# Kernel tuning notes

Hardware: AMD Instinct MI355X
Metric: run time of the kernel (lower is better)

The kernel has to match this reference:

```python
import jax, jax.numpy as jnp
import numpy as np

B, H, W = 4, 64, 64
DIM, NH, HD = 768, 12, 64
MLP_DIM = 3072
WS = 14
EPS = 1e-6
SCALE = HD ** -0.5
QMIN, QMAX = -128.0, 127.0  # 8-bit signed fake-quant range


def fake_quant(x, s):
    # uniform quant-dequant with straight-through estimator
    q = jnp.clip(jnp.round(x / s), QMIN, QMAX) * s
    return x + jax.lax.stop_gradient(q - x)


def layer_norm(x, w, b):
    mu = jnp.mean(x, axis=-1, keepdims=True)
    var = jnp.var(x, axis=-1, keepdims=True)
    return (x - mu) * jax.lax.rsqrt(var + EPS) * w + b


def qlinear(x, w, b, a_s, w_s):
    # PreQuantizedLayer: fake-quant input activation and weight, then linear
    return fake_quant(x, a_s) @ fake_quant(w, w_s).T + b


def _attention(xw, qkv_w, qkv_b, proj_w, proj_b, rel_pos_h, rel_pos_w, a_s, w_s):
    Bw = xw.shape[0]
    N = WS * WS
    qkv = qlinear(xw.reshape(Bw, N, DIM), qkv_w, qkv_b, a_s[4], w_s[0])
    qkv = qkv.reshape(Bw, N, 3, NH, HD).transpose(2, 0, 3, 1, 4).reshape(3, Bw * NH, N, HD)
    q = fake_quant(qkv[0], a_s[0])
    k = fake_quant(qkv[1], a_s[1])
    v = fake_quant(qkv[2], a_s[2])
    attn = jnp.einsum('bqc,bkc->bqk', q * SCALE, k)  # (Bw*NH, N, N)
    # decomposed relative position bias (q_size == k_size == WS)
    idx = jnp.arange(WS)[:, None] - jnp.arange(WS)[None, :] + (WS - 1)
    Rh = rel_pos_h[idx]  # (WS, WS, HD)
    Rw = rel_pos_w[idx]
    r_q = q.reshape(Bw * NH, WS, WS, HD)
    rel_h = jnp.einsum('bhwc,hkc->bhwk', r_q, Rh)
    rel_w = jnp.einsum('bhwc,wkc->bhwk', r_q, Rw)
    attn = (attn.reshape(-1, WS, WS, WS, WS) + rel_h[..., :, None] + rel_w[..., None, :]).reshape(-1, N, N)
    attn = fake_quant(jax.nn.softmax(attn, axis=-1), a_s[3])
    out = jnp.einsum('bqk,bkc->bqc', attn, v)
    out = out.reshape(Bw, NH, WS, WS, HD).transpose(0, 2, 3, 1, 4).reshape(Bw, WS, WS, DIM)
    return qlinear(out, proj_w, proj_b, a_s[5], w_s[1])


def _forward(x, ln1_w, ln1_b, ln2_w, ln2_b, qkv_w, qkv_b, proj_w, proj_b,
             lin1_w, lin1_b, lin2_w, lin2_b, rel_pos_h, rel_pos_w, act_scales, w_scales):
    shortcut = x
    h = layer_norm(x, ln1_w, ln1_b)
    pad_h = (WS - H % WS) % WS
    pad_w = (WS - W % WS) % WS
    Hp, Wp = H + pad_h, W + pad_w
    hp = jnp.pad(h, ((0, 0), (0, pad_h), (0, pad_w), (0, 0)))
    win = hp.reshape(B, Hp // WS, WS, Wp // WS, WS, DIM).transpose(0, 1, 3, 2, 4, 5).reshape(-1, WS, WS, DIM)
    win = _attention(win, qkv_w, qkv_b, proj_w, proj_b, rel_pos_h, rel_pos_w, act_scales, w_scales)
    hp = win.reshape(B, Hp // WS, Wp // WS, WS, WS, DIM).transpose(0, 1, 3, 2, 4, 5).reshape(B, Hp, Wp, DIM)
    x = shortcut + hp[:, :H, :W, :]
    y = layer_norm(x, ln2_w, ln2_b)
    y = qlinear(y, lin1_w, lin1_b, act_scales[6], w_scales[2])
    y = jax.nn.gelu(y, approximate=False)
    y = qlinear(y, lin2_w, lin2_b, act_scales[7], w_scales[3])
    return x + y


def setup_inputs() -> dict:
    key = jax.random.key(0)
    ks = jax.random.split(key, 12)
    def w(k, shape, std=0.02):
        return jax.random.normal(k, shape, dtype=jnp.float32) * std
    return {
        'x': jax.random.normal(ks[0], (B, H, W, DIM), dtype=jnp.float32),
        'ln1_w': jnp.ones((DIM,), jnp.float32), 'ln1_b': jnp.zeros((DIM,), jnp.float32),
        'ln2_w': jnp.ones((DIM,), jnp.float32), 'ln2_b': jnp.zeros((DIM,), jnp.float32),
        'qkv_w': w(ks[1], (3 * DIM, DIM)), 'qkv_b': jnp.zeros((3 * DIM,), jnp.float32),
        'proj_w': w(ks[2], (DIM, DIM)), 'proj_b': jnp.zeros((DIM,), jnp.float32),
        'lin1_w': w(ks[3], (MLP_DIM, DIM)), 'lin1_b': jnp.zeros((MLP_DIM,), jnp.float32),
        'lin2_w': w(ks[4], (DIM, MLP_DIM)), 'lin2_b': jnp.zeros((DIM,), jnp.float32),
        'rel_pos_h': w(ks[5], (2 * WS - 1, HD)), 'rel_pos_w': w(ks[6], (2 * WS - 1, HD)),
        'act_scales': jax.random.uniform(ks[7], (8,), jnp.float32, 0.01, 0.06),
        'w_scales': jax.random.uniform(ks[8], (4,), jnp.float32, 0.0005, 0.003),
    }


def reference(x, ln1_w, ln1_b, ln2_w, ln2_b, qkv_w, qkv_b, proj_w, proj_b,
              lin1_w, lin1_b, lin2_w, lin2_b, rel_pos_h, rel_pos_w, act_scales, w_scales):
    return _forward(x, ln1_w, ln1_b, ln2_w, ln2_b, qkv_w, qkv_b, proj_w, proj_b,
                    lin1_w, lin1_b, lin2_w, lin2_b, rel_pos_h, rel_pos_w, act_scales, w_scales)
```

## Files before the change

kernel.cpp:

```cpp
#include <hip/hip_runtime.h>
#include <cstdint>


typedef int   v4i __attribute__((ext_vector_type(4)));
typedef float v4f __attribute__((ext_vector_type(4)));
typedef short v8s __attribute__((ext_vector_type(8)));
typedef int8_t i8;

__device__ __forceinline__ i8 satq(float x) {
  float q = rintf(x);
  q = fminf(127.f, fmaxf(-128.f, q));
  return (i8)(int)q;
}

__device__ __forceinline__ void gload16(const i8* g, i8* l) {
  __builtin_amdgcn_global_load_lds((const __attribute__((address_space(1))) void*)g,
                                   (__attribute__((address_space(3))) void*)l, 16, 0, 0);
}

__device__ __forceinline__ int pack4(const i8* q) {
  return ((int)(unsigned char)q[0]) | ((int)(unsigned char)q[1] << 8) |
         ((int)(unsigned char)q[2] << 16) | ((int)(unsigned char)q[3] << 24);
}

__device__ __forceinline__ float fast_gelu(float v) {
  float x = fabsf(v) * 0.70710678118654752f;
  float t = __builtin_amdgcn_rcpf(fmaf(0.3275911f, x, 1.0f));
  float s = fmaf(1.061405429f, t, -1.453152027f);
  s = fmaf(s, t, 1.421413741f);
  s = fmaf(s, t, -0.284496736f);
  s = fmaf(s, t, 0.254829592f);
  s = s * t;
  float e = __expf(-x * x);
  float erfa = fmaf(-s, e, 1.0f);
  float erfs = copysignf(erfa, v);
  float hv = 0.5f * v;
  return fmaf(hv, erfs, hv);
}

__global__ __launch_bounds__(256) void k_prep(const float* __restrict__ qkvw,
    const float* __restrict__ projw, const float* __restrict__ lin1w,
    const float* __restrict__ lin2w, i8* __restrict__ wqb,
    const float* __restrict__ rph, const float* __restrict__ rpw,
    short* __restrict__ TB, const float* __restrict__ wsc) {
  int b = blockIdx.x;
  if (b < 1728) {
    int i = b * 256 + threadIdx.x;
    const float* w; int base, sidx;
    if (i < 110592)      { w = qkvw;  base = 0;      sidx = 0; }
    else if (i < 147456) { w = projw; base = 110592; sidx = 1; }
    else if (i < 294912) { w = lin1w; base = 147456; sidx = 2; }
    else                 { w = lin2w; base = 294912; sidx = 3; }
    float inv = 1.0f / wsc[sidx];
    const float4* src = (const float4*)w + (size_t)(i - base) * 4;
    i8 buf[16];
#pragma unroll
    for (int t = 0; t < 4; t++) {
      float4 f = src[t];
      buf[t*4+0] = satq(f.x * inv); buf[t*4+1] = satq(f.y * inv);
      buf[t*4+2] = satq(f.z * inv); buf[t*4+3] = satq(f.w * inv);
    }
    *(v4i*)(wqb + (size_t)i * 16) = *(v4i*)buf;
  } else {
    int g = (b - 1728) * 256 + threadIdx.x;
    int lane = g & 63, c = g >> 6;
    int p = c & 1, ks = (c >> 1) & 1, nt = (c >> 2) & 1, tb = c >> 3;
    const float* src = tb ? rpw : rph;
    int n = nt * 16 + (lane & 15);
    int k0 = ks * 32 + (lane >> 4) * 8;
    short outv[8];
#pragma unroll
    for (int j = 0; j < 8; j++) {
      float v = (n < 27) ? src[n * 64 + k0 + j] : 0.f;
      unsigned u = __float_as_uint(v);
      unsigned hi = (u + 0x7fffu + ((u >> 16) & 1u)) >> 16;
      if (p == 0) outv[j] = (short)hi;
      else {
        float lof = v - __uint_as_float(hi << 16);
        unsigned ul = __float_as_uint(lof);
        outv[j] = (short)((ul + 0x7fffu + ((ul >> 16) & 1u)) >> 16);
      }
    }
    *(v8s*)(TB + (size_t)c * 512 + lane * 8) = *(v8s*)outv;
  }
}

__global__ __launch_bounds__(256) void k_ln1(const float* __restrict__ x,
    const float* __restrict__ w, const float* __restrict__ b,
    const float* __restrict__ as, i8* __restrict__ outq) {
  int wt = blockIdx.x * 4 + (threadIdx.x >> 6);
  int lane = threadIdx.x & 63;
  int win = wt / 196, tok = wt - win * 196;
  int bb = win / 25, wrem = win - bb * 25, wh = wrem / 5, ww = wrem - wh * 5;
  int r = tok / 14, c = tok - r * 14;
  int y = wh * 14 + r, xx = ww * 14 + c;
  i8* dst = outq + (size_t)wt * 768 + lane * 12;
  if (y >= 64 || xx >= 64) {
    ((int*)dst)[0] = 0; ((int*)dst)[1] = 0; ((int*)dst)[2] = 0;
    return;
  }
  const float* row = x + (((size_t)bb * 64 + y) * 64 + xx) * 768 + lane * 12;
  float v[12];
  *(float4*)(v)     = *(const float4*)(row);
  *(float4*)(v + 4) = *(const float4*)(row + 4);
  *(float4*)(v + 8) = *(const float4*)(row + 8);
  float s = 0.f, ss = 0.f;
#pragma unroll
  for (int j = 0; j < 12; j++) { s += v[j]; ss += v[j] * v[j]; }
#pragma unroll
  for (int off = 1; off < 64; off <<= 1) { s += __shfl_xor(s, off); ss += __shfl_xor(ss, off); }
  float mu = s * (1.0f / 768.0f);
  float var = ss * (1.0f / 768.0f) - mu * mu;
  float rstd = 1.0f / sqrtf(var + 1e-6f);
  float inv = 1.0f / as[4];
  float wv[12], bv[12];
  *(float4*)(wv)     = *(const float4*)(w + lane * 12);
  *(float4*)(wv + 4) = *(const float4*)(w + lane * 12 + 4);
  *(float4*)(wv + 8) = *(const float4*)(w + lane * 12 + 8);
  *(float4*)(bv)     = *(const float4*)(b + lane * 12);
  *(float4*)(bv + 4) = *(const float4*)(b + lane * 12 + 4);
  *(float4*)(bv + 8) = *(const float4*)(b + lane * 12 + 8);
  i8 q[12];
#pragma unroll
  for (int j = 0; j < 12; j++) q[j] = satq(((v[j] - mu) * rstd * wv[j] + bv[j]) * inv);
  ((int*)dst)[0] = pack4(q); ((int*)dst)[1] = pack4(q + 4); ((int*)dst)[2] = pack4(q + 8);
}

__global__ __launch_bounds__(256) void k_ln2(const float* __restrict__ x2,
    const float* __restrict__ w, const float* __restrict__ b,
    const float* __restrict__ as, i8* __restrict__ outq) {
  int tokg = blockIdx.x * 4 + (threadIdx.x >> 6);
  int lane = threadIdx.x & 63;
  const float* row = x2 + (size_t)tokg * 768 + lane * 12;
  float v[12];
  *(float4*)(v)     = *(const float4*)(row);
  *(float4*)(v + 4) = *(const float4*)(row + 4);
  *(float4*)(v + 8) = *(const float4*)(row + 8);
  float s = 0.f, ss = 0.f;
#pragma unroll
  for (int j = 0; j < 12; j++) { s += v[j]; ss += v[j] * v[j]; }
#pragma unroll
  for (int off = 1; off < 64; off <<= 1) { s += __shfl_xor(s, off); ss += __shfl_xor(ss, off); }
  float mu = s * (1.0f / 768.0f);
  float var = ss * (1.0f / 768.0f) - mu * mu;
  float rstd = 1.0f / sqrtf(var + 1e-6f);
  float inv = 1.0f / as[6];
  float wv[12], bv[12];
  *(float4*)(wv)     = *(const float4*)(w + lane * 12);
  *(float4*)(wv + 4) = *(const float4*)(w + lane * 12 + 4);
  *(float4*)(wv + 8) = *(const float4*)(w + lane * 12 + 8);
  *(float4*)(bv)     = *(const float4*)(b + lane * 12);
  *(float4*)(bv + 4) = *(const float4*)(b + lane * 12 + 4);
  *(float4*)(bv + 8) = *(const float4*)(b + lane * 12 + 8);
  i8* dst = outq + (size_t)tokg * 768 + lane * 12;
  i8 q[12];
#pragma unroll
  for (int j = 0; j < 12; j++) q[j] = satq(((v[j] - mu) * rstd * wv[j] + bv[j]) * inv);
  ((int*)dst)[0] = pack4(q); ((int*)dst)[1] = pack4(q + 4); ((int*)dst)[2] = pack4(q + 8);
}

template <class Epi>
__global__ __launch_bounds__(256) void k_gemm(const i8* __restrict__ A, const i8* __restrict__ B,
                                              int M, int N, int K, Epi epi) {
  __shared__ __align__(16) i8 As[3][8192];
  __shared__ __align__(16) i8 Bs[3][8192];
  const int tid = threadIdx.x;
  const int lane = tid & 63, wave = tid >> 6;
  const int quad = lane >> 4, lc = lane & 15;
  const int wr = wave >> 1, wc = wave & 1;
  const long bm = (long)blockIdx.y * 128, bn = (long)blockIdx.x * 128;
  const v4i vz = {0, 0, 0, 0};
  v4i acc[4][4];
#pragma unroll
  for (int i = 0; i < 4; i++)
#pragma unroll
    for (int j = 0; j < 4; j++) acc[i][j] = vz;

  const int r0 = tid >> 2, c0 = tid & 3;
  const int cs = c0 ^ ((r0 >> 1) & 3);
  long rA0 = bm + r0;      if (rA0 >= M) rA0 = 0;
  long rA1 = bm + r0 + 64; if (rA1 >= M) rA1 = 0;
  const i8* pA0 = A + rA0 * (size_t)K + cs * 16;
  const i8* pA1 = A + rA1 * (size_t)K + cs * 16;
  const i8* pB0 = B + (bn + r0)      * (size_t)K + cs * 16;
  const i8* pB1 = B + (bn + r0 + 64) * (size_t)K + cs * 16;

  auto stage = [&](int buf) {
    gload16(pA0, As[buf] + tid * 16); gload16(pA1, As[buf] + 4096 + tid * 16);
    gload16(pB0, Bs[buf] + tid * 16); gload16(pB1, Bs[buf] + 4096 + tid * 16);
    pA0 += 64; pA1 += 64; pB0 += 64; pB1 += 64;
  };

  const int xq16 = (quad ^ ((lc >> 1) & 3)) * 16;

  auto compute = [&](int buf) {
    v4i af[4], bf[4];
#pragma unroll
    for (int i = 0; i < 4; i++) af[i] = *(const v4i*)(As[buf] + (wr * 64 + i * 16 + lc) * 64 + xq16);
#pragma unroll
    for (int j = 0; j < 4; j++) bf[j] = *(const v4i*)(Bs[buf] + (wc * 64 + j * 16 + lc) * 64 + xq16);
#pragma unroll
    for (int i = 0; i < 4; i++)
#pragma unroll
      for (int j = 0; j < 4; j++)
        acc[i][j] = __builtin_amdgcn_mfma_i32_16x16x64_i8(bf[j], af[i], acc[i][j], 0, 0, 0);
  };

  const int nt = K >> 6;
  stage(0); stage(1);
  int cb = 0, sb = 2;
  for (int t = 0; t < nt - 1; ++t) {
    asm volatile("s_waitcnt vmcnt(4)" ::: "memory");
    __builtin_amdgcn_s_barrier();
    asm volatile("" ::: "memory");
    if (t + 2 < nt) { stage(sb); if (++sb == 3) sb = 0; }
    compute(cb); if (++cb == 3) cb = 0;
  }
  asm volatile("s_waitcnt vmcnt(0)" ::: "memory");
  __builtin_amdgcn_s_barrier();
  asm volatile("" ::: "memory");
  compute(cb);

  Epi e = epi;
  e.init();
#pragma unroll
  for (int i = 0; i < 4; i++) {
    int gm = (int)bm + wr * 64 + i * 16 + lc;
#pragma unroll
    for (int j = 0; j < 4; j++) {
      int gn0 = (int)bn + wc * 64 + j * 16 + quad * 4;
      if (gm < M) e.store4(acc[i][j], gm, gn0);
    }
  }
}

struct EpiQKV {
  const float* as; const float* wsc; const float* bias;
  i8 *qq, *kq, *vt;
  float sab, invq, invk, invv;
  __device__ void init() {
    sab = as[4] * wsc[0]; invq = 1.f / as[0]; invk = 1.f / as[1]; invv = 1.f / as[2];
  }
  __device__ void store4(const v4i a, int m, int n0) {
    int t = n0 / 768, rem = n0 - t * 768;
    int head = rem >> 6, ch0 = rem & 63;
    int win = m / 196, tok = m - win * 196;
    size_t bh = (size_t)win * 12 + head;
    float4 bv = *(const float4*)(bias + n0);
    const float* bp = (const float*)&bv;
    if (t == 2) {
#pragma unroll
      for (int r = 0; r < 4; r++)
        vt[(bh * 64 + ch0 + r) * 256 + tok] = satq(((float)a[r] * sab + bp[r]) * invv);
    } else {
      float inv = (t == 0) ? invq : invk;
      i8 q[4];
#pragma unroll
      for (int r = 0; r < 4; r++) q[r] = satq(((float)a[r] * sab + bp[r]) * inv);
      *(int*)((t == 0 ? qq : kq) + (bh * 196 + tok) * 64 + ch0) = pack4(q);
    }
  }
};

struct EpiProj {
  const float* as; const float* wsc; const float* bias; const float* x0; float* out;
  float sab;
  __device__ void init() { sab = as[5] * wsc[1]; }
  __device__ void store4(const v4i a, int m, int n0) {
    int win = m / 196, tok = m - win * 196;
    int bb = win / 25, wrem = win - bb * 25, wh = wrem / 5, ww = wrem - wh * 5;
    int rr = tok / 14, cc = tok - rr * 14;
    int y = wh * 14 + rr, xx = ww * 14 + cc;
    if (y >= 64 || xx >= 64) return;
    size_t o = (((size_t)bb * 64 + y) * 64 + xx) * 768 + n0;
    float4 bv = *(const float4*)(bias + n0);
    float4 xv = *(const float4*)(x0 + o);
    float4 ov;
    ov.x = (float)a[0] * sab + bv.x + xv.x;
    ov.y = (float)a[1] * sab + bv.y + xv.y;
    ov.z = (float)a[2] * sab + bv.z + xv.z;
    ov.w = (float)a[3] * sab + bv.w + xv.w;
    *(float4*)(out + o) = ov;
  }
};

struct EpiLin1 {
  const float* as; const float* wsc; const float* bias; i8* outq;
  float sab, invg;
  __device__ void init() { sab = as[6] * wsc[2]; invg = 1.f / as[7]; }
  __device__ void store4(const v4i a, int m, int n0) {
    float4 bv = *(const float4*)(bias + n0);
    const float* bp = (const float*)&bv;
    i8 q[4];
#pragma unroll
    for (int r = 0; r < 4; r++) {
      float v = fmaf((float)a[r], sab, bp[r]);
      q[r] = satq(fast_gelu(v) * invg);
    }
    *(int*)(outq + (size_t)m * 3072 + n0) = pack4(q);
  }
};

struct EpiLin2 {
  const float* as; const float* wsc; const float* bias; float* out;
  float sab;
  __device__ void init() { sab = as[7] * wsc[3]; }
  __device__ void store4(const v4i a, int m, int n0) {
    size_t o = (size_t)m * 768 + n0;
    float4 bv = *(const float4*)(bias + n0);
    float4 ov = *(const float4*)(out + o);
    ov.x += (float)a[0] * sab + bv.x;
    ov.y += (float)a[1] * sab + bv.y;
    ov.z += (float)a[2] * sab + bv.z;
    ov.w += (float)a[3] * sab + bv.w;
    *(float4*)(out + o) = ov;
  }
};

__global__ __launch_bounds__(64, 4) void k_attn(const i8* __restrict__ qq, const i8* __restrict__ kq,
    const i8* __restrict__ vt, const short* __restrict__ TB,
    const float* __restrict__ as, i8* __restrict__ outq) {
  __shared__ float relS[16][66];
  const int g = blockIdx.x;
  const int work = (g & 7) * 1950 + (g >> 3);
  const int bh = work / 13;
  const int t = work - bh * 13;
  const int win = bh / 12, head = bh - win * 12;
  const int lane = threadIdx.x;
  const int quad = lane >> 4, lc = lane & 15;
  const float s0 = as[0];
  const float ssc = s0 * as[1] * 0.125f;
  const float invs3 = 1.0f / as[3];
  const float oscale = as[2] * as[3] / as[5];

  const v8s* TBv = (const v8s*)TB;
  const v4i vz = {0, 0, 0, 0};

  {
    int arow = t * 16 + lc; if (arow > 195) arow = 195;
    const i8* qrow = qq + ((size_t)bh * 196 + arow) * 64;
    v8s af[2];
#pragma unroll
    for (int ks = 0; ks < 2; ks++) {
      const i8* p = qrow + ks * 32 + quad * 8;
#pragma unroll
      for (int j = 0; j < 8; j++)
        af[ks][j] = (short)(__float_as_uint((float)p[j]) >> 16);
    }
    v4f rh0 = {0,0,0,0}, rh1 = {0,0,0,0}, rw0 = {0,0,0,0}, rw1 = {0,0,0,0};
#pragma unroll
    for (int ks = 0; ks < 2; ks++)
#pragma unroll
      for (int p2 = 0; p2 < 2; p2++) {
        rh0 = __builtin_amdgcn_mfma_f32_16x16x32_bf16(af[ks], TBv[(0*4 + ks*2 + p2)*64 + lane], rh0, 0, 0, 0);
        rh1 = __builtin_amdgcn_mfma_f32_16x16x32_bf16(af[ks], TBv[(1*4 + ks*2 + p2)*64 + lane], rh1, 0, 0, 0);
        rw0 = __builtin_amdgcn_mfma_f32_16x16x32_bf16(af[ks], TBv[(2*4 + ks*2 + p2)*64 + lane], rw0, 0, 0, 0);
        rw1 = __builtin_amdgcn_mfma_f32_16x16x32_bf16(af[ks], TBv[(3*4 + ks*2 + p2)*64 + lane], rw1, 0, 0, 0);
      }
#pragma unroll
    for (int r = 0; r < 4; r++) {
      int rl = quad * 4 + r;
      relS[rl][lc]      = rh0[r] * s0;
      relS[rl][16 + lc] = rh1[r] * s0;
      relS[rl][32 + lc] = rw0[r] * s0;
      relS[rl][48 + lc] = rw1[r] * s0;
    }
  }

  v4i aq = *(const v4i*)(qq + ((size_t)bh * 196 + t * 16 + lc) * 64 + quad * 16);
  v4i sacc[13];
#pragma unroll
  for (int f = 0; f < 13; f++) {
    v4i bk = *(const v4i*)(kq + ((size_t)bh * 196 + f * 16 + lc) * 64 + quad * 16);
    sacc[f] = __builtin_amdgcn_mfma_i32_16x16x64_i8(bk, aq, vz, 0, 0, 0);
  }

  unsigned khw[13];
#pragma unroll
  for (int f = 0; f < 13; f++) {
    unsigned w0 = 0, w1 = 0, w2 = 0, w3 = 0;
#pragma unroll
    for (int r = 0; r < 4; r++) {
      int k0 = f*16 + 0*4 + r; if (k0 > 195) k0 = 195;
      int k1 = f*16 + 1*4 + r; if (k1 > 195) k1 = 195;
      int k2 = f*16 + 2*4 + r; if (k2 > 195) k2 = 195;
      int k3 = f*16 + 3*4 + r; if (k3 > 195) k3 = 195;
      w0 |= (unsigned)(((k0/14) << 4) | (k0 - (k0/14)*14)) << (r*8);
      w1 |= (unsigned)(((k1/14) << 4) | (k1 - (k1/14)*14)) << (r*8);
      w2 |= (unsigned)(((k2/14) << 4) | (k2 - (k2/14)*14)) << (r*8);
      w3 |= (unsigned)(((k3/14) << 4) | (k3 - (k3/14)*14)) << (r*8);
    }
    khw[f] = quad == 0 ? w0 : quad == 1 ? w1 : quad == 2 ? w2 : w3;
  }

  int qrow = t * 16 + lc;
  int qh = qrow / 14, qw = qrow - qh * 14;
  const float* rH = &relS[lc][13 + qh];
  const float* rW = &relS[lc][32 + 13 + qw];
  float L[13][4];
  float mx = -1e30f;
#pragma unroll
  for (int f = 0; f < 13; f++)
#pragma unroll
    for (int r = 0; r < 4; r++) {
      int kh = (int)((khw[f] >> (r * 8 + 4)) & 0xfu);
      int kw = (int)((khw[f] >> (r * 8)) & 0xfu);
      float v = ((f < 12) | (quad == 0))
                  ? fmaf((float)sacc[f][r], ssc, rH[-kh] + rW[-kw]) : -1e30f;
      L[f][r] = v;
      mx = fmaxf(mx, v);
    }
  mx = fmaxf(mx, __shfl_xor(mx, 16));
  mx = fmaxf(mx, __shfl_xor(mx, 32));
  float sum = 0.f;
#pragma unroll
  for (int f = 0; f < 13; f++)
#pragma unroll
    for (int r = 0; r < 4; r++) { float e = __expf(L[f][r] - mx); L[f][r] = e; sum += e; }
  sum += __shfl_xor(sum, 16);
  sum += __shfl_xor(sum, 32);
  float cq = (1.0f / sum) * invs3;

  unsigned W[16];
#pragma unroll
  for (int f = 0; f < 13; f++) {
    i8 q4[4];
#pragma unroll
    for (int r = 0; r < 4; r++) q4[r] = satq(L[f][r] * cq);
    W[f] = (unsigned)pack4(q4);
  }
  W[13] = 0; W[14] = 0; W[15] = 0;

  v4i oacc[4];
#pragma unroll
  for (int nt = 0; nt < 4; nt++) oacc[nt] = vz;
  const bool q0m = (quad & 1) == 0, q1m = (quad & 2) == 0;
#pragma unroll
  for (int kc = 0; kc < 4; kc++) {
    unsigned a0 = W[kc*4+0], a1 = W[kc*4+1], a2 = W[kc*4+2], a3 = W[kc*4+3];
    unsigned s0_ = (unsigned)__shfl_xor((int)a1, 16);
    unsigned s1_ = (unsigned)__shfl_xor((int)a0, 16);
    unsigned s2_ = (unsigned)__shfl_xor((int)a3, 16);
    unsigned s3_ = (unsigned)__shfl_xor((int)a2, 16);
    unsigned x0 = q0m ? a0 : s0_;
    unsigned x1 = q0m ? s1_ : a1;
    unsigned x2 = q0m ? a2 : s2_;
    unsigned x3 = q0m ? s3_ : a3;
    unsigned u0 = (unsigned)__shfl_xor((int)x2, 32);
    unsigned u1 = (unsigned)__shfl_xor((int)x3, 32);
    unsigned u2 = (unsigned)__shfl_xor((int)x0, 32);
    unsigned u3 = (unsigned)__shfl_xor((int)x1, 32);
    v4i ap;
    ap[0] = (int)(q1m ? x0 : u0);
    ap[1] = (int)(q1m ? x1 : u1);
    ap[2] = (int)(q1m ? u2 : x2);
    ap[3] = (int)(q1m ? u3 : x3);
#pragma unroll
    for (int nt = 0; nt < 4; nt++) {
      v4i bv = *(const v4i*)(vt + ((size_t)bh * 64 + nt * 16 + lc) * 256 + kc * 64 + quad * 16);
      oacc[nt] = __builtin_amdgcn_mfma_i32_16x16x64_i8(bv, ap, oacc[nt], 0, 0, 0);
    }
  }
  if (t * 16 + lc < 196) {
    i8* orow = outq + ((size_t)win * 196 + t * 16 + lc) * 768 + head * 64 + quad * 4;
#pragma unroll
    for (int nt = 0; nt < 4; nt++) {
      i8 q4[4];
#pragma unroll
      for (int r = 0; r < 4; r++) q4[r] = satq((float)oacc[nt][r] * oscale);
      *(int*)(orow + nt * 16) = pack4(q4);
    }
  }
}

extern "C" void kernel_launch(void* const* d_in, const int* in_sizes, int n_in,
                              void* d_out, int out_size, void* d_ws, size_t ws_size,
                              hipStream_t stream) {
  const float* x     = (const float*)d_in[0];
  const float* ln1w  = (const float*)d_in[1];
  const float* ln1b  = (const float*)d_in[2];
  const float* ln2w  = (const float*)d_in[3];
  const float* ln2b  = (const float*)d_in[4];
  const float* qkvw  = (const float*)d_in[5];
  const float* qkvb  = (const float*)d_in[6];
  const float* projw = (const float*)d_in[7];
  const float* projb = (const float*)d_in[8];
  const float* lin1w = (const float*)d_in[9];
  const float* lin1b = (const float*)d_in[10];
  const float* lin2w = (const float*)d_in[11];
  const float* lin2b = (const float*)d_in[12];
  const float* rph   = (const float*)d_in[13];
  const float* rpw   = (const float*)d_in[14];
  const float* as    = (const float*)d_in[15];
  const float* wsc   = (const float*)d_in[16];
  float* out = (float*)d_out;

  char* ws = (char*)d_ws;
  i8* big    = (i8*)ws;
  i8* qq     = big;
  i8* kq     = big + 15052800;
  i8* vt     = big + 30105600;
  short* TB  = (short*)(big + 49766400);
  i8* mlpq   = big;
  i8* creg   = (i8*)(ws + 50331648);
  i8* winq   = creg;
  i8* attno  = creg;
  i8* yq     = creg;
  i8* wqb    = (i8*)(ws + 65384448);
  i8* qkvwq  = wqb;
  i8* projwq = wqb + 1769472;
  i8* lin1wq = projwq + 589824;
  i8* lin2wq = lin1wq + 2359296;

  k_prep<<<1732, 256, 0, stream>>>(qkvw, projw, lin1w, lin2w, wqb, rph, rpw, TB, wsc);

  k_ln1<<<4900, 256, 0, stream>>>(x, ln1w, ln1b, as, winq);

  { EpiQKV e{as, wsc, qkvb, qq, kq, vt};
    k_gemm<EpiQKV><<<dim3(18, 154), 256, 0, stream>>>(winq, qkvwq, 19600, 2304, 768, e); }

  k_attn<<<15600, 64, 0, stream>>>(qq, kq, vt, TB, as, attno);

  { EpiProj e{as, wsc, projb, x, out};
    k_gemm<EpiProj><<<dim3(6, 154), 256, 0, stream>>>(attno, projwq, 19600, 768, 768, e); }

  k_ln2<<<4096, 256, 0, stream>>>(out, ln2w, ln2b, as, yq);

  { EpiLin1 e{as, wsc, lin1b, mlpq};
    k_gemm<EpiLin1><<<dim3(24, 128), 256, 0, stream>>>(yq, lin1wq, 16384, 3072, 768, e); }

  { EpiLin2 e{as, wsc, lin2b, out};
    k_gemm<EpiLin2><<<dim3(6, 128), 256, 0, stream>>>(mlpq, lin2wq, 16384, 768, 3072, e); }
}
```

Measured before the change: 517.5 us.

## Store attention output head-major and read it strided in proj GEMM

The attention kernel now transposes its quantized output in registers with lane shuffles, so each lane writes 16 contiguous bytes into a head-major [window*head, token, 64] layout. Before, each lane wrote four scattered 4-byte stores into the token-major 768-wide row. The proj GEMM gets an AHEAD template mode that indexes A in this layout, stepping by one head block per K tile. This trades narrow scattered global writes for wide stores, at the cost of extra shuffles and a less contiguous A-tile read pattern in the GEMM.

```diff
diff --git a/kernel.cpp b/kernel.cpp
--- a/kernel.cpp
+++ b/kernel.cpp
@@ -159,7 +159,7 @@
   ((int*)dst)[0] = pack4(q); ((int*)dst)[1] = pack4(q + 4); ((int*)dst)[2] = pack4(q + 8);
 }
 
-template <class Epi>
+template <class Epi, bool AHEAD = false>
 __global__ __launch_bounds__(256) void k_gemm(const i8* __restrict__ A, const i8* __restrict__ B,
                                               int M, int N, int K, Epi epi) {
   __shared__ __align__(16) i8 As[3][8192];
@@ -180,15 +180,26 @@
   const int cs = c0 ^ ((r0 >> 1) & 3);
   long rA0 = bm + r0;      if (rA0 >= M) rA0 = 0;
   long rA1 = bm + r0 + 64; if (rA1 >= M) rA1 = 0;
-  const i8* pA0 = A + rA0 * (size_t)K + cs * 16;
-  const i8* pA1 = A + rA1 * (size_t)K + cs * 16;
+  const i8 *pA0, *pA1;
+  long astep;
+  if (AHEAD) {
+    long w0 = rA0 / 196, t0 = rA0 - w0 * 196;
+    long w1 = rA1 / 196, t1 = rA1 - w1 * 196;
+    pA0 = A + (w0 * 2352 + t0) * 64 + cs * 16;
+    pA1 = A + (w1 * 2352 + t1) * 64 + cs * 16;
+    astep = 196 * 64;
+  } else {
+    pA0 = A + rA0 * (size_t)K + cs * 16;
+    pA1 = A + rA1 * (size_t)K + cs * 16;
+    astep = 64;
+  }
   const i8* pB0 = B + (bn + r0)      * (size_t)K + cs * 16;
   const i8* pB1 = B + (bn + r0 + 64) * (size_t)K + cs * 16;
 
   auto stage = [&](int buf) {
     gload16(pA0, As[buf] + tid * 16); gload16(pA1, As[buf] + 4096 + tid * 16);
     gload16(pB0, Bs[buf] + tid * 16); gload16(pB1, Bs[buf] + 4096 + tid * 16);
-    pA0 += 64; pA1 += 64; pB0 += 64; pB1 += 64;
+    pA0 += astep; pA1 += astep; pB0 += 64; pB1 += 64;
   };
 
   const int xq16 = (quad ^ ((lc >> 1) & 3)) * 16;
@@ -325,7 +336,7 @@
   const int work = (g & 7) * 1950 + (g >> 3);
   const int bh = work / 13;
   const int t = work - bh * 13;
-  const int win = bh / 12, head = bh - win * 12;
+  const int win = bh / 12;
   const int lane = threadIdx.x;
   const int quad = lane >> 4, lc = lane & 15;
   const float s0 = as[0];
@@ -431,10 +442,11 @@
   }
   W[13] = 0; W[14] = 0; W[15] = 0;
 
+  const bool q0m = (quad & 1) == 0, q1m = (quad & 2) == 0;
+
   v4i oacc[4];
 #pragma unroll
   for (int nt = 0; nt < 4; nt++) oacc[nt] = vz;
-  const bool q0m = (quad & 1) == 0, q1m = (quad & 2) == 0;
 #pragma unroll
   for (int kc = 0; kc < 4; kc++) {
     unsigned a0 = W[kc*4+0], a1 = W[kc*4+1], a2 = W[kc*4+2], a3 = W[kc*4+3];
@@ -461,15 +473,36 @@
       oacc[nt] = __builtin_amdgcn_mfma_i32_16x16x64_i8(bv, ap, oacc[nt], 0, 0, 0);
     }
   }
-  if (t * 16 + lc < 196) {
-    i8* orow = outq + ((size_t)win * 196 + t * 16 + lc) * 768 + head * 64 + quad * 4;
-#pragma unroll
-    for (int nt = 0; nt < 4; nt++) {
-      i8 q4[4];
-#pragma unroll
-      for (int r = 0; r < 4; r++) q4[r] = satq((float)oacc[nt][r] * oscale);
-      *(int*)(orow + nt * 16) = pack4(q4);
-    }
+
+  unsigned W2[4];
+#pragma unroll
+  for (int nt = 0; nt < 4; nt++) {
+    i8 q4[4];
+#pragma unroll
+    for (int r = 0; r < 4; r++) q4[r] = satq((float)oacc[nt][r] * oscale);
+    W2[nt] = (unsigned)pack4(q4);
+  }
+  {
+    unsigned a0 = W2[0], a1 = W2[1], a2 = W2[2], a3 = W2[3];
+    unsigned s0_ = (unsigned)__shfl_xor((int)a1, 16);
+    unsigned s1_ = (unsigned)__shfl_xor((int)a0, 16);
+    unsigned s2_ = (unsigned)__shfl_xor((int)a3, 16);
+    unsigned s3_ = (unsigned)__shfl_xor((int)a2, 16);
+    unsigned x0 = q0m ? a0 : s0_;
+    unsigned x1 = q0m ? s1_ : a1;
+    unsigned x2 = q0m ? a2 : s2_;
+    unsigned x3 = q0m ? s3_ : a3;
+    unsigned u0 = (unsigned)__shfl_xor((int)x2, 32);
+    unsigned u1 = (unsigned)__shfl_xor((int)x3, 32);
+    unsigned u2 = (unsigned)__shfl_xor((int)x0, 32);
+    unsigned u3 = (unsigned)__shfl_xor((int)x1, 32);
+    v4i ot;
+    ot[0] = (int)(q1m ? x0 : u0);
+    ot[1] = (int)(q1m ? x1 : u1);
+    ot[2] = (int)(q1m ? u2 : x2);
+    ot[3] = (int)(q1m ? u3 : x3);
+    if (t * 16 + lc < 196)
+      *(v4i*)(outq + ((size_t)bh * 196 + t * 16 + lc) * 64 + quad * 16) = ot;
   }
 }
 
@@ -522,7 +555,7 @@
   k_attn<<<15600, 64, 0, stream>>>(qq, kq, vt, TB, as, attno);
 
   { EpiProj e{as, wsc, projb, x, out};
-    k_gemm<EpiProj><<<dim3(6, 154), 256, 0, stream>>>(attno, projwq, 19600, 768, 768, e); }
+    k_gemm<EpiProj, true><<<dim3(6, 154), 256, 0, stream>>>(attno, projwq, 19600, 768, 768, e); }
 
   k_ln2<<<4096, 256, 0, stream>>>(out, ln2w, ln2b, as, yq);
 
```

New measurement: 509.3 us. No clear change (-1.6%).
